# Performance work log

Measured on AMD Instinct MI355X. Metric: run time of the kernel, lower is better.

## Reference

```python
import jax, jax.numpy as jnp
import numpy as np

B, S, IN_DIM, OUT_DIM, HID = 16, 256, 128, 128, 512


def setup_inputs() -> dict:
    key = jax.random.key(0)
    ks = jax.random.split(key, 7)
    x = jax.random.normal(ks[0], (B, S, IN_DIM), dtype=jnp.float32)
    # hypernet linear 1: input_dim -> hyper_hidden_dim
    W1 = jax.random.normal(ks[1], (IN_DIM, HID), dtype=jnp.float32) / np.sqrt(IN_DIM)
    b1 = jax.random.normal(ks[2], (HID,), dtype=jnp.float32) * 0.01
    # hypernet linear 2: hyper_hidden_dim -> input_dim * output_dim
    W2 = jax.random.normal(ks[3], (HID, IN_DIM * OUT_DIM), dtype=jnp.float32) / np.sqrt(HID)
    b2 = jax.random.normal(ks[4], (IN_DIM * OUT_DIM,), dtype=jnp.float32) * 0.01
    # final fc: output_dim -> output_dim
    Wfc = jax.random.normal(ks[5], (OUT_DIM, OUT_DIM), dtype=jnp.float32) / np.sqrt(OUT_DIM)
    bfc = jax.random.normal(ks[6], (OUT_DIM,), dtype=jnp.float32) * 0.01
    return {"x": x, "W1": W1, "b1": b1, "W2": W2, "b2": b2, "Wfc": Wfc, "bfc": bfc}


def reference(x, W1, b1, W2, b2, Wfc, bfc):
    # hypernet: per-token generated weight matrix Wx [B,S,IN,OUT]
    h = jax.nn.relu(jnp.einsum('bsi,ih->bsh', x, W1) + b1)
    Wx = (jnp.einsum('bsh,ho->bso', h, W2) + b2).reshape(x.shape[0], x.shape[1], IN_DIM, OUT_DIM)
    # batched vector-matrix product per (b,s), then sum over s -> [B, OUT]
    y = jnp.einsum('bsi,bsio->bo', x, Wx)
    return y @ Wfc + bfc
```

## Files before the change

### kernel.cpp

```cpp
#include <hip/hip_runtime.h>


typedef __attribute__((ext_vector_type(8))) short     s16x8;
typedef __attribute__((ext_vector_type(8))) unsigned short u16x8;
typedef __attribute__((ext_vector_type(4))) float     f32x4;

__device__ __forceinline__ unsigned short f2bf(float f) {
    union { float f; unsigned int u; } v; v.f = f;
    unsigned int r = v.u + 0x7FFFu + ((v.u >> 16) & 1u);
    return (unsigned short)(r >> 16);
}
__device__ __forceinline__ float bf2f(unsigned short u) {
    union { unsigned int u; float f; } v; v.u = ((unsigned int)u) << 16;
    return v.f;
}

#define OFF_MP   0
#define OFF_PART 2097152
#define OFF_SXP  3145728

__global__ __launch_bounds__(256) void k_AB(const float* __restrict__ x,
        const float* __restrict__ W1, const float* __restrict__ b1,
        float* __restrict__ Mp, float* __restrict__ sxp) {
    __shared__ __align__(16) unsigned char smem[87296];
    auto Ws  = (unsigned short (*)[136])(smem);
    auto xA  = (unsigned short (*)[136])(smem + 17408);
    auto xTl = (unsigned short (*)[136])(smem + 52224);
    auto Wt  = (float (*)[33])(smem + 52224);
    float* b1s = (float*)(smem + 87040);
    auto hts = (unsigned short (*)[136])(smem);

    const int tid = threadIdx.x;
    const int b  = blockIdx.x >> 4;
    const int hb = (blockIdx.x >> 1) & 7;
    const int sh = blockIdx.x & 1;

    {
        const int r = tid >> 1, q = tid & 1;
        const float* xrow = &x[(size_t)(b * 256 + sh * 128 + r) * 128 + q * 64];
        #pragma unroll
        for (int m = 0; m < 8; ++m) {
            const float4 v0 = *(const float4*)&xrow[m * 8];
            const float4 v1 = *(const float4*)&xrow[m * 8 + 4];
            unsigned short t8[8] __attribute__((aligned(16))) = {
                f2bf(v0.x), f2bf(v0.y), f2bf(v0.z), f2bf(v0.w),
                f2bf(v1.x), f2bf(v1.y), f2bf(v1.z), f2bf(v1.w)};
            *(u16x8*)&xA[r][q * 64 + m * 8] = *(u16x8*)t8;
        }
        if (tid < 64) b1s[tid] = b1[hb * 64 + tid];
    }
    for (int hq = 0; hq < 2; ++hq) {
        __syncthreads();
        #pragma unroll
        for (int p = 0; p < 16; ++p) {
            const int flat = p * 256 + tid;
            const int i = flat >> 5, hc = flat & 31;
            Wt[i][hc] = W1[(size_t)i * 512 + hb * 64 + hq * 32 + hc];
        }
        __syncthreads();
        {
            const int h2 = tid >> 3, pt = tid & 7;
            unsigned short t16[16] __attribute__((aligned(16)));
            #pragma unroll
            for (int m = 0; m < 16; ++m)
                t16[m] = f2bf(Wt[pt * 16 + m][h2]);
            *(u16x8*)&Ws[hq * 32 + h2][pt * 16]     = *(u16x8*)&t16[0];
            *(u16x8*)&Ws[hq * 32 + h2][pt * 16 + 8] = *(u16x8*)&t16[8];
        }
    }
    __syncthreads();

    const int w = tid >> 6, lane = tid & 63;
    const int wr = w >> 1, wc = w & 1;
    const int l15 = lane & 15, kl = lane >> 4;
    f32x4 zero = {0.f, 0.f, 0.f, 0.f};

    f32x4 acc[4][2];
    #pragma unroll
    for (int i = 0; i < 4; ++i)
        #pragma unroll
        for (int j = 0; j < 2; ++j) acc[i][j] = zero;
    #pragma unroll
    for (int ks = 0; ks < 4; ++ks) {
        s16x8 a[4], bb[2];
        #pragma unroll
        for (int f = 0; f < 4; ++f)
            a[f] = *(const s16x8*)&xA[wr * 64 + f * 16 + l15][ks * 32 + kl * 8];
        #pragma unroll
        for (int f = 0; f < 2; ++f)
            bb[f] = *(const s16x8*)&Ws[wc * 32 + f * 16 + l15][ks * 32 + kl * 8];
        #pragma unroll
        for (int fr = 0; fr < 4; ++fr)
            #pragma unroll
            for (int fc = 0; fc < 2; ++fc)
                acc[fr][fc] = __builtin_amdgcn_mfma_f32_16x16x32_bf16(a[fr], bb[fc], acc[fr][fc], 0, 0, 0);
    }
    __syncthreads();

    {
        const int i = tid >> 1, q = tid & 1;
        float sacc = 0.f;
        unsigned short t64[64] __attribute__((aligned(16)));
        #pragma unroll
        for (int m = 0; m < 64; ++m) {
            const unsigned short u = xA[q * 64 + m][i];
            sacc += bf2f(u);
            t64[m] = u;
        }
        #pragma unroll
        for (int v = 0; v < 8; ++v)
            *(u16x8*)&xTl[i][q * 64 + v * 8] = *(u16x8*)&t64[v * 8];
        if (hb == 0)
            sxp[(size_t)((sh * 2 + q) * 16 + b) * 128 + i] = sacc;
    }
    __syncthreads();

    #pragma unroll
    for (int fr = 0; fr < 4; ++fr)
        #pragma unroll
        for (int fc = 0; fc < 2; ++fc)
            #pragma unroll
            for (int j = 0; j < 4; ++j) {
                const int tok = wr * 64 + fr * 16 + kl * 4 + j;
                const int hid = wc * 32 + fc * 16 + l15;
                const float v = acc[fr][fc][j] + b1s[hid];
                hts[hid][tok] = f2bf(v > 0.f ? v : 0.f);
            }
    __syncthreads();

    f32x4 acc2[2][4];
    #pragma unroll
    for (int i = 0; i < 2; ++i)
        #pragma unroll
        for (int j = 0; j < 4; ++j) acc2[i][j] = zero;
    #pragma unroll
    for (int ks = 0; ks < 4; ++ks) {
        s16x8 a2[2], b2f[4];
        #pragma unroll
        for (int f = 0; f < 2; ++f)
            a2[f] = *(const s16x8*)&hts[wr * 32 + f * 16 + l15][ks * 32 + kl * 8];
        #pragma unroll
        for (int f = 0; f < 4; ++f)
            b2f[f] = *(const s16x8*)&xTl[wc * 64 + f * 16 + l15][ks * 32 + kl * 8];
        #pragma unroll
        for (int fr = 0; fr < 2; ++fr)
            #pragma unroll
            for (int fc = 0; fc < 4; ++fc)
                acc2[fr][fc] = __builtin_amdgcn_mfma_f32_16x16x32_bf16(a2[fr], b2f[fc], acc2[fr][fc], 0, 0, 0);
    }
    const size_t mpbase = (size_t)(sh * 16 + b) * 65536;
    #pragma unroll
    for (int fr = 0; fr < 2; ++fr)
        #pragma unroll
        for (int fc = 0; fc < 4; ++fc)
            #pragma unroll
            for (int j = 0; j < 4; ++j) {
                const int h = hb * 64 + wr * 32 + fr * 16 + kl * 4 + j;
                const int i = wc * 64 + fc * 16 + l15;
                Mp[mpbase + (size_t)h * 128 + i] = acc2[fr][fc][j];
            }
}

__global__ __launch_bounds__(256) void k_C(const float* __restrict__ Mp,
        const float* __restrict__ W2, float* __restrict__ part) {
    __shared__ float Ms[16][128];
    const int tid = threadIdx.x;
    const int p = blockIdx.x;
    const int k0 = p * 128;
    #pragma unroll
    for (int r = 0; r < 8; ++r) {
        const int flat = r * 256 + tid;
        const int b = flat >> 7, kk = flat & 127;
        Ms[b][kk] = Mp[(size_t)b * 65536 + k0 + kk]
                  + Mp[(size_t)(16 + b) * 65536 + k0 + kk];
    }
    __syncthreads();
    const int lane = tid & 63;
    const int wb   = tid >> 6;
    const int o2   = lane * 2;
    float2 acc[4] = {{0.f,0.f},{0.f,0.f},{0.f,0.f},{0.f,0.f}};
    float2 wbuf[8];
    for (int kb = 0; kb < 128; kb += 8) {
        #pragma unroll
        for (int u = 0; u < 8; ++u)
            wbuf[u] = *(const float2*)&W2[(size_t)(k0 + kb + u) * 128 + o2];
        #pragma unroll
        for (int u = 0; u < 8; ++u) {
            #pragma unroll
            for (int bb = 0; bb < 4; ++bb) {
                const float m = Ms[wb * 4 + bb][kb + u];
                acc[bb].x += m * wbuf[u].x;
                acc[bb].y += m * wbuf[u].y;
            }
        }
    }
    #pragma unroll
    for (int bb = 0; bb < 4; ++bb)
        *(float2*)&part[(size_t)(p * 16 + wb * 4 + bb) * 128 + o2] = acc[bb];
}

__global__ __launch_bounds__(1024) void k_D(const float* __restrict__ part,
        const float* __restrict__ sxp, const float* __restrict__ b2,
        const float* __restrict__ Wfc, const float* __restrict__ bfc,
        float* __restrict__ out) {
    __shared__ float sh[8][128];
    __shared__ float sxs[128];
    __shared__ float ysum[128];
    __shared__ float ysh[128];
    const int b = blockIdx.x;
    const int t = threadIdx.x & 127;
    const int g = threadIdx.x >> 7;
    float y = 0.f;
    #pragma unroll 8
    for (int pp = g * 64; pp < g * 64 + 64; ++pp)
        y += part[(size_t)(pp * 16 + b) * 128 + t];
    sh[g][t] = y;
    __syncthreads();
    if (g == 0) {
        float yy = sh[0][t];
        #pragma unroll
        for (int j = 1; j < 8; ++j) yy += sh[j][t];
        ysum[t] = yy;
        sxs[t] = sxp[(size_t)(0 * 16 + b) * 128 + t] + sxp[(size_t)(1 * 16 + b) * 128 + t]
               + sxp[(size_t)(2 * 16 + b) * 128 + t] + sxp[(size_t)(3 * 16 + b) * 128 + t];
    }
    __syncthreads();
    float yb = 0.f;
    #pragma unroll
    for (int i = g * 16; i < g * 16 + 16; ++i)
        yb += sxs[i] * b2[i * 128 + t];
    sh[g][t] = yb;
    __syncthreads();
    if (g == 0) {
        float yy = ysum[t];
        #pragma unroll
        for (int j = 0; j < 8; ++j) yy += sh[j][t];
        ysh[t] = yy;
    }
    __syncthreads();
    float f = 0.f;
    #pragma unroll
    for (int oo = g * 16; oo < g * 16 + 16; ++oo)
        f += ysh[oo] * Wfc[oo * 128 + t];
    sh[g][t] = f;
    __syncthreads();
    if (g == 0) {
        float s = bfc[t];
        #pragma unroll
        for (int j = 0; j < 8; ++j) s += sh[j][t];
        out[b * 128 + t] = s;
    }
}

extern "C" void kernel_launch(void* const* d_in, const int* in_sizes, int n_in,
                              void* d_out, int out_size, void* d_ws, size_t ws_size,
                              hipStream_t stream) {
    const float* x   = (const float*)d_in[0];
    const float* W1  = (const float*)d_in[1];
    const float* b1  = (const float*)d_in[2];
    const float* W2  = (const float*)d_in[3];
    const float* b2  = (const float*)d_in[4];
    const float* Wfc = (const float*)d_in[5];
    const float* bfc = (const float*)d_in[6];
    float* ws  = (float*)d_ws;
    float* Mp   = ws + OFF_MP;
    float* part = ws + OFF_PART;
    float* sxp  = ws + OFF_SXP;
    float* out  = (float*)d_out;

    k_AB<<<256, 256, 0, stream>>>(x, W1, b1, Mp, sxp);
    k_C <<<512, 256, 0, stream>>>(Mp, W2, part);
    k_D <<<16, 1024, 0, stream>>>(part, sxp, b2, Wfc, bfc, out);
}
```

Measured before the change: 31.94 us.

## Split k_C reduction across lane groups with float4 W2 loads and shuffle reduce

Reworks the k_C inner GEMV so each wavefront splits the 128-long K dimension into four 32-wide slices, one per 16-lane group. Each lane now owns 8 output columns and loads W2 with float4 instead of float2, and the M values are read as float4 from a padded LDS layout to avoid bank conflicts. Partial sums are combined with xor shuffles and only one lane group writes results. This aims to cut the serial loop length and raise memory-level parallelism on W2 streaming, at the cost of more registers and extra shuffle work.

```diff
diff --git a/kernel.cpp b/kernel.cpp
--- a/kernel.cpp
+++ b/kernel.cpp
@@ -163,7 +163,7 @@
 
 __global__ __launch_bounds__(256) void k_C(const float* __restrict__ Mp,
         const float* __restrict__ W2, float* __restrict__ part) {
-    __shared__ float Ms[16][128];
+    __shared__ float Msl[16][144];
     const int tid = threadIdx.x;
     const int p = blockIdx.x;
     const int k0 = p * 128;
@@ -171,32 +171,56 @@
     for (int r = 0; r < 8; ++r) {
         const int flat = r * 256 + tid;
         const int b = flat >> 7, kk = flat & 127;
-        Ms[b][kk] = Mp[(size_t)b * 65536 + k0 + kk]
-                  + Mp[(size_t)(16 + b) * 65536 + k0 + kk];
-    }
-    __syncthreads();
-    const int lane = tid & 63;
-    const int wb   = tid >> 6;
-    const int o2   = lane * 2;
-    float2 acc[4] = {{0.f,0.f},{0.f,0.f},{0.f,0.f},{0.f,0.f}};
-    float2 wbuf[8];
-    for (int kb = 0; kb < 128; kb += 8) {
-        #pragma unroll
-        for (int u = 0; u < 8; ++u)
-            wbuf[u] = *(const float2*)&W2[(size_t)(k0 + kb + u) * 128 + o2];
-        #pragma unroll
-        for (int u = 0; u < 8; ++u) {
+        Msl[b][36 * (kk >> 5) + (kk & 31)] =
+            Mp[(size_t)b * 65536 + k0 + kk] + Mp[(size_t)(16 + b) * 65536 + k0 + kk];
+    }
+    __syncthreads();
+    const int lane = tid & 63, wb = tid >> 6;
+    const int kpar = lane >> 4, og = lane & 15;
+    const int o8 = og * 8;
+    float acc[4][8] = {};
+    for (int ib = 0; ib < 8; ++ib) {
+        float4 wst[8];
+        #pragma unroll
+        for (int j = 0; j < 4; ++j) {
+            const size_t row = (size_t)(k0 + kpar * 32 + ib * 4 + j) * 128;
+            wst[j * 2]     = *(const float4*)&W2[row + o8];
+            wst[j * 2 + 1] = *(const float4*)&W2[row + o8 + 4];
+        }
+        float4 mv[4];
+        #pragma unroll
+        for (int bb = 0; bb < 4; ++bb)
+            mv[bb] = *(const float4*)&Msl[wb * 4 + bb][36 * kpar + ib * 4];
+        #pragma unroll
+        for (int j = 0; j < 4; ++j) {
+            const float4 w0 = wst[j * 2], w1 = wst[j * 2 + 1];
             #pragma unroll
             for (int bb = 0; bb < 4; ++bb) {
-                const float m = Ms[wb * 4 + bb][kb + u];
-                acc[bb].x += m * wbuf[u].x;
-                acc[bb].y += m * wbuf[u].y;
+                const float m = ((const float*)&mv[bb])[j];
+                acc[bb][0] += m * w0.x; acc[bb][1] += m * w0.y;
+                acc[bb][2] += m * w0.z; acc[bb][3] += m * w0.w;
+                acc[bb][4] += m * w1.x; acc[bb][5] += m * w1.y;
+                acc[bb][6] += m * w1.z; acc[bb][7] += m * w1.w;
             }
         }
     }
     #pragma unroll
     for (int bb = 0; bb < 4; ++bb)
-        *(float2*)&part[(size_t)(p * 16 + wb * 4 + bb) * 128 + o2] = acc[bb];
+        #pragma unroll
+        for (int o = 0; o < 8; ++o) {
+            acc[bb][o] += __shfl_xor(acc[bb][o], 16);
+            acc[bb][o] += __shfl_xor(acc[bb][o], 32);
+        }
+    if (kpar == 0) {
+        #pragma unroll
+        for (int bb = 0; bb < 4; ++bb) {
+            float4 v0 = {acc[bb][0], acc[bb][1], acc[bb][2], acc[bb][3]};
+            float4 v1 = {acc[bb][4], acc[bb][5], acc[bb][6], acc[bb][7]};
+            float* dst = &part[(size_t)(p * 16 + wb * 4 + bb) * 128 + o8];
+            *(float4*)dst = v0;
+            *(float4*)(dst + 4) = v1;
+        }
+    }
 }
 
 __global__ __launch_bounds__(1024) void k_D(const float* __restrict__ part,
```

Measured after the change: 33.95 us. +6.3%, slower.
